# Performance work log

Hardware: AMD Instinct MI355X
Metric: run time of the kernel (lower is better)

The kernel has to match this reference:

```python
import jax, jax.numpy as jnp
import numpy as np

B, S, D, K = 4, 8192, 512, 20


def setup_inputs() -> dict:
    key = jax.random.key(0)
    k1, k2, k3, k4 = jax.random.split(key, 4)
    std = 0.02  # _init_weights: normal(0, 0.02/sqrt(layer_idx+1)), layer_idx=0
    return {
        "x": jax.random.normal(k1, (B, S, D), dtype=jnp.float32),
        "positions": jax.random.normal(k2, (K, D), dtype=jnp.float32) * 0.2,
        "log_scales": jnp.log(1.0 + 0.5 * jax.random.uniform(k3, (K,), dtype=jnp.float32)),
        "amplitudes": 1.2 + 0.3 * jax.random.uniform(k4, (K,), dtype=jnp.float32),
        "w_v": jax.random.normal(jax.random.fold_in(key, 10), (D, D), dtype=jnp.float32) * std,
        "w_o": jax.random.normal(jax.random.fold_in(key, 11), (D, D), dtype=jnp.float32) * std,
    }


def reference(x, positions, log_scales, amplitudes, w_v, w_o):
    # Gaussian-splat RBF attention (token -> splat -> token routing).
    scales = jnp.exp(log_scales)  # [K]
    # squared distances ||x - c||^2 via expansion (avoids [B,S,K,D] tensor)
    x2 = jnp.sum(x * x, axis=-1, keepdims=True)           # [B,S,1]
    c2 = jnp.sum(positions * positions, axis=-1)          # [K]
    xc = jnp.einsum('bsd,kd->bsk', x, positions)          # [B,S,K]
    d2 = jnp.maximum(x2 - 2.0 * xc + c2, 0.0)             # [B,S,K]
    gauss = amplitudes * jnp.exp(-0.5 * d2 / (scales * scales))  # [B,S,K]
    attn = gauss / (jnp.sum(gauss, axis=-1, keepdims=True) + 1e-8)  # per-token normalize
    v = jnp.einsum('bsd,ed->bse', x, w_v)                 # token_value_proj (no bias)
    splat_states = jnp.einsum('bsk,bsd->bkd', attn, v)    # gather token values at splats
    out = jnp.einsum('bsk,bkd->bsd', attn, splat_states)  # scatter back to tokens
    return jnp.einsum('bsd,ed->bse', out, w_o)            # output_proj (dropout=eval identity)
```

## Files before the change

### kernel.cpp

```cpp
#include <hip/hip_runtime.h>
#include <hip/hip_bf16.h>

#define BB 4
#define SS 8192
#define DD 512
#define KK 20
#define CHUNKS 64

__global__ void k0_params(const float* __restrict__ pos,
                          const float* __restrict__ log_scales,
                          const float* __restrict__ amps,
                          float* __restrict__ params) {
  int k = blockIdx.x;
  int lane = threadIdx.x;
  float acc = 0.f;
  for (int d = lane; d < DD; d += 64) { float p = pos[k * DD + d]; acc += p * p; }
#pragma unroll
  for (int off = 32; off > 0; off >>= 1) acc += __shfl_xor(acc, off);
  if (lane == 0) {
    params[k] = acc;
    float s = __expf(log_scales[k]);
    params[KK + k] = 0.5f / (s * s);
    params[2 * KK + k] = amps[k];
  }
}

__global__ __launch_bounds__(256) void k1_attn(
    const float* __restrict__ x, const float* __restrict__ pos,
    const float* __restrict__ params, float* __restrict__ attn) {
  __shared__ float pos_s[KK * DD];
  int tid = threadIdx.x;
  for (int i = tid; i < KK * DD / 4; i += 256)
    ((float4*)pos_s)[i] = ((const float4*)pos)[i];
  __syncthreads();

  int tl = tid >> 2;
  int dsub = tid & 3;
  size_t tok = (size_t)blockIdx.x * 64 + tl;
  const float* xrow = x + tok * DD;

  float acc[KK];
#pragma unroll
  for (int k = 0; k < KK; ++k) acc[k] = 0.f;
  float x2 = 0.f;

#pragma unroll 4
  for (int j = 0; j < 32; ++j) {
    int d0 = j * 16 + dsub * 4;
    float4 xv = *(const float4*)(xrow + d0);
    x2 += xv.x * xv.x + xv.y * xv.y + xv.z * xv.z + xv.w * xv.w;
#pragma unroll
    for (int k = 0; k < KK; ++k) {
      float4 p = *(const float4*)(pos_s + k * DD + d0);
      acc[k] += xv.x * p.x + xv.y * p.y + xv.z * p.z + xv.w * p.w;
    }
  }
#pragma unroll
  for (int k = 0; k < KK; ++k) {
    acc[k] += __shfl_xor(acc[k], 1);
    acc[k] += __shfl_xor(acc[k], 2);
  }
  x2 += __shfl_xor(x2, 1);
  x2 += __shfl_xor(x2, 2);

  if (dsub == 0) {
    float g[KK];
    float sum = 0.f;
#pragma unroll
    for (int k = 0; k < KK; ++k) {
      float d2 = fmaxf(x2 - 2.f * acc[k] + params[k], 0.f);
      float gk = params[2 * KK + k] * __expf(-params[KK + k] * d2);
      g[k] = gk;
      sum += gk;
    }
    float inv = 1.f / (sum + 1e-8f);
    float* arow = attn + tok * KK;
#pragma unroll
    for (int k = 0; k < KK; ++k) arow[k] = g[k] * inv;
  }
}

__global__ __launch_bounds__(256) void k2_scatter(
    const float* __restrict__ x, const float* __restrict__ attn,
    float* __restrict__ Mpart) {
  int t = threadIdx.x;
  int c = blockIdx.x;
  int b = blockIdx.y;
  int s0 = c * (SS / CHUNKS);

  float2 Ml[KK];
#pragma unroll
  for (int k = 0; k < KK; ++k) Ml[k] = make_float2(0.f, 0.f);

  for (int s = s0; s < s0 + SS / CHUNKS; ++s) {
    size_t tokb = (size_t)b * SS + s;
    float2 xv = *(const float2*)(x + tokb * DD + 2 * t);
    const float* arow = attn + tokb * KK;
#pragma unroll
    for (int k = 0; k < KK; ++k) {
      float a = arow[k];
      Ml[k].x += a * xv.x;
      Ml[k].y += a * xv.y;
    }
  }
  float* base = Mpart + (((size_t)b * CHUNKS + c) * KK) * DD + 2 * t;
#pragma unroll
  for (int k = 0; k < KK; ++k)
    *(float2*)(base + (size_t)k * DD) = Ml[k];
}

__global__ __launch_bounds__(256) void k2b_reduce(
    const float* __restrict__ Mpart, float* __restrict__ Mg) {
  int idx = blockIdx.x * 256 + threadIdx.x;
  int b = idx / (KK * DD);
  int kd = idx - b * (KK * DD);
  const float* p = Mpart + (size_t)b * CHUNKS * KK * DD + kd;
  float acc = 0.f;
#pragma unroll 8
  for (int c = 0; c < CHUNKS; ++c) acc += p[(size_t)c * KK * DD];
  Mg[idx] = acc;
}

__global__ __launch_bounds__(256) void k3_proj(
    const float* __restrict__ in, const float* __restrict__ W,
    float* __restrict__ out) {
  __shared__ float row_s[DD];
  int bk = blockIdx.x;
  int t = threadIdx.x;
  for (int i = t; i < DD / 4; i += 256)
    ((float4*)row_s)[i] = ((const float4*)(in + (size_t)bk * DD))[i];
  __syncthreads();
  int e = blockIdx.y * 256 + t;
  const float* wrow = W + (size_t)e * DD;
  float acc = 0.f;
#pragma unroll 4
  for (int j = 0; j < DD / 4; ++j) {
    float4 w4 = *(const float4*)(wrow + 4 * j);
    float4 m4 = ((const float4*)row_s)[j];
    acc += m4.x * w4.x + m4.y * w4.y + m4.z * w4.z + m4.w * w4.w;
  }
  out[(size_t)bk * DD + e] = acc;
}

__global__ __launch_bounds__(256) void k5_gather(
    const float* __restrict__ attn, const float* __restrict__ ws2,
    float* __restrict__ out) {
  int t = threadIdx.x;
  int b = blockIdx.y;
  int s0 = blockIdx.x * (SS / CHUNKS);

  float2 w[KK];
#pragma unroll
  for (int k = 0; k < KK; ++k)
    w[k] = *(const float2*)(ws2 + ((size_t)b * KK + k) * DD + 2 * t);

  for (int s = s0; s < s0 + SS / CHUNKS; ++s) {
    size_t tokb = (size_t)b * SS + s;
    const float* arow = attn + tokb * KK;
    float2 o = make_float2(0.f, 0.f);
#pragma unroll
    for (int k = 0; k < KK; ++k) {
      float a = arow[k];
      o.x += a * w[k].x;
      o.y += a * w[k].y;
    }
    *(float2*)(out + tokb * DD + 2 * t) = o;
  }
}

extern "C" void kernel_launch(void* const* d_in, const int* in_sizes, int n_in,
                              void* d_out, int out_size, void* d_ws, size_t ws_size,
                              hipStream_t stream) {
  const float* x   = (const float*)d_in[0];
  const float* pos = (const float*)d_in[1];
  const float* ls  = (const float*)d_in[2];
  const float* am  = (const float*)d_in[3];
  const float* w_v = (const float*)d_in[4];
  const float* w_o = (const float*)d_in[5];
  float* out = (float*)d_out;

  float* ws     = (float*)d_ws;
  float* params = ws;
  float* attn   = ws + 64;
  float* Mg     = attn + (size_t)BB * SS * KK;
  float* ssb    = Mg + (size_t)BB * KK * DD;
  float* ws2    = ssb + (size_t)BB * KK * DD;
  float* Mpart  = ws2 + (size_t)BB * KK * DD;

  k0_params<<<KK, 64, 0, stream>>>(pos, ls, am, params);
  k1_attn<<<(BB * SS) / 64, 256, 0, stream>>>(x, pos, params, attn);
  k2_scatter<<<dim3(CHUNKS, BB), 256, 0, stream>>>(x, attn, Mpart);
  k2b_reduce<<<(BB * KK * DD) / 256, 256, 0, stream>>>(Mpart, Mg);
  k3_proj<<<dim3(BB * KK, 2), 256, 0, stream>>>(Mg, w_v, ssb);
  k3_proj<<<dim3(BB * KK, 2), 256, 0, stream>>>(ssb, w_o, ws2);
  k5_gather<<<dim3(CHUNKS, BB), 256, 0, stream>>>(attn, ws2, out);
}
```

Measured before the change: 250.6 us.

## Fuse attention, scatter and projections into fewer kernels with per-tile partials

Merges the parameter, attention and scatter stages into one kernel that computes splat weights for 64-token tiles in shared memory, then immediately accumulates per-tile splat partial sums from the same x rows. The two projections and the chunk reduction are folded into a single 512-thread kernel, and the gather kernel now stages attention rows in shared memory with more, smaller blocks. This cuts kernel launches and avoids a second full read of x for the scatter. In exchange it writes many more partial sums (128 chunks per batch), and keeps a fallback path for when the workspace is too small.

```diff
diff --git a/kernel.cpp b/kernel.cpp
--- a/kernel.cpp
+++ b/kernel.cpp
@@ -5,166 +5,231 @@
 #define SS 8192
 #define DD 512
 #define KK 20
-#define CHUNKS 64
-
-__global__ void k0_params(const float* __restrict__ pos,
-                          const float* __restrict__ log_scales,
-                          const float* __restrict__ amps,
-                          float* __restrict__ params) {
-  int k = blockIdx.x;
-  int lane = threadIdx.x;
-  float acc = 0.f;
-  for (int d = lane; d < DD; d += 64) { float p = pos[k * DD + d]; acc += p * p; }
-#pragma unroll
-  for (int off = 32; off > 0; off >>= 1) acc += __shfl_xor(acc, off);
-  if (lane == 0) {
-    params[k] = acc;
-    float s = __expf(log_scales[k]);
-    params[KK + k] = 0.5f / (s * s);
-    params[2 * KK + k] = amps[k];
-  }
-}
-
-__global__ __launch_bounds__(256) void k1_attn(
+#define TT 64
+#define CPB1 (SS / TT)
+#define CPB2 64
+
+__device__ __forceinline__ float dot4(float4 a, float4 b) {
+  return a.x * b.x + a.y * b.y + a.z * b.z + a.w * b.w;
+}
+
+__global__ __launch_bounds__(256) void k12_fused(
     const float* __restrict__ x, const float* __restrict__ pos,
-    const float* __restrict__ params, float* __restrict__ attn) {
+    const float* __restrict__ log_scales, const float* __restrict__ amps,
+    float* __restrict__ attn_g, float* __restrict__ Mpart, int doM) {
   __shared__ float pos_s[KK * DD];
+  __shared__ float attn_s[TT * KK];
+  __shared__ float prm_s[3 * KK];
+
   int tid = threadIdx.x;
+  int blk = blockIdx.x;
+  int b = blk >> 7;
+  int c = blk & 127;
+  size_t row0 = (size_t)b * SS + (size_t)c * TT;
+
   for (int i = tid; i < KK * DD / 4; i += 256)
     ((float4*)pos_s)[i] = ((const float4*)pos)[i];
   __syncthreads();
 
-  int tl = tid >> 2;
-  int dsub = tid & 3;
-  size_t tok = (size_t)blockIdx.x * 64 + tl;
-  const float* xrow = x + tok * DD;
-
-  float acc[KK];
-#pragma unroll
-  for (int k = 0; k < KK; ++k) acc[k] = 0.f;
-  float x2 = 0.f;
-
-#pragma unroll 4
-  for (int j = 0; j < 32; ++j) {
-    int d0 = j * 16 + dsub * 4;
-    float4 xv = *(const float4*)(xrow + d0);
-    x2 += xv.x * xv.x + xv.y * xv.y + xv.z * xv.z + xv.w * xv.w;
+  if (tid < KK * 8) {
+    int k = tid >> 3, i = tid & 7;
+    float a = 0.f;
+    const float4* pr = (const float4*)(pos_s + k * DD);
+#pragma unroll
+    for (int j = 0; j < 16; ++j) {
+      float4 p = pr[i * 16 + j];
+      a += dot4(p, p);
+    }
+    a += __shfl_xor(a, 1); a += __shfl_xor(a, 2); a += __shfl_xor(a, 4);
+    if (i == 0) {
+      prm_s[k] = a;
+      float s = __expf(log_scales[k]);
+      prm_s[KK + k] = 0.5f / (s * s);
+      prm_s[2 * KK + k] = amps[k];
+    }
+  }
+  __syncthreads();
+
+  int q = tid >> 4;
+  int dsub = tid & 15;
+  const float* xq = x + (row0 + q) * DD;
+
+  float acc[4][KK];
+  float x2[4];
+#pragma unroll
+  for (int r = 0; r < 4; ++r) {
+    x2[r] = 0.f;
+#pragma unroll
+    for (int k = 0; k < KK; ++k) acc[r][k] = 0.f;
+  }
+
+  for (int j = 0; j < 8; ++j) {
+    int d0 = j * 64 + dsub * 4;
+    float4 xv[4];
+#pragma unroll
+    for (int r = 0; r < 4; ++r) xv[r] = *(const float4*)(xq + (size_t)r * 16 * DD + d0);
+#pragma unroll
+    for (int r = 0; r < 4; ++r) x2[r] += dot4(xv[r], xv[r]);
 #pragma unroll
     for (int k = 0; k < KK; ++k) {
       float4 p = *(const float4*)(pos_s + k * DD + d0);
-      acc[k] += xv.x * p.x + xv.y * p.y + xv.z * p.z + xv.w * p.w;
-    }
-  }
-#pragma unroll
-  for (int k = 0; k < KK; ++k) {
-    acc[k] += __shfl_xor(acc[k], 1);
-    acc[k] += __shfl_xor(acc[k], 2);
-  }
-  x2 += __shfl_xor(x2, 1);
-  x2 += __shfl_xor(x2, 2);
+#pragma unroll
+      for (int r = 0; r < 4; ++r) acc[r][k] += dot4(xv[r], p);
+    }
+  }
+
+#pragma unroll
+  for (int r = 0; r < 4; ++r) {
+    x2[r] += __shfl_xor(x2[r], 1); x2[r] += __shfl_xor(x2[r], 2);
+    x2[r] += __shfl_xor(x2[r], 4); x2[r] += __shfl_xor(x2[r], 8);
+#pragma unroll
+    for (int k = 0; k < KK; ++k) {
+      float v = acc[r][k];
+      v += __shfl_xor(v, 1); v += __shfl_xor(v, 2);
+      v += __shfl_xor(v, 4); v += __shfl_xor(v, 8);
+      acc[r][k] = v;
+    }
+  }
 
   if (dsub == 0) {
-    float g[KK];
-    float sum = 0.f;
-#pragma unroll
-    for (int k = 0; k < KK; ++k) {
-      float d2 = fmaxf(x2 - 2.f * acc[k] + params[k], 0.f);
-      float gk = params[2 * KK + k] * __expf(-params[KK + k] * d2);
-      g[k] = gk;
-      sum += gk;
-    }
-    float inv = 1.f / (sum + 1e-8f);
-    float* arow = attn + tok * KK;
-#pragma unroll
-    for (int k = 0; k < KK; ++k) arow[k] = g[k] * inv;
-  }
-}
-
-__global__ __launch_bounds__(256) void k2_scatter(
+#pragma unroll
+    for (int r = 0; r < 4; ++r) {
+      float g[KK];
+      float sum = 0.f;
+#pragma unroll
+      for (int k = 0; k < KK; ++k) {
+        float d2 = fmaxf(x2[r] - 2.f * acc[r][k] + prm_s[k], 0.f);
+        float gk = prm_s[2 * KK + k] * __expf(-prm_s[KK + k] * d2);
+        g[k] = gk;
+        sum += gk;
+      }
+      float inv = 1.f / (sum + 1e-8f);
+      float* as = attn_s + (q + r * 16) * KK;
+#pragma unroll
+      for (int k = 0; k < KK; ++k) as[k] = g[k] * inv;
+    }
+  }
+  __syncthreads();
+
+  {
+    float* ag = attn_g + row0 * KK;
+    for (int i = tid; i < TT * KK; i += 256) ag[i] = attn_s[i];
+  }
+
+  if (!doM) return;
+
+  float2 Ml[KK];
+#pragma unroll
+  for (int k = 0; k < KK; ++k) Ml[k] = make_float2(0.f, 0.f);
+
+  const float* xb = x + row0 * DD + 2 * tid;
+  for (int s = 0; s < TT; ++s) {
+    float2 xv = *(const float2*)(xb + (size_t)s * DD);
+    const float4* ar4 = (const float4*)(attn_s + s * KK);
+#pragma unroll
+    for (int kk = 0; kk < KK / 4; ++kk) {
+      float4 a4 = ar4[kk];
+      Ml[4 * kk + 0].x += a4.x * xv.x; Ml[4 * kk + 0].y += a4.x * xv.y;
+      Ml[4 * kk + 1].x += a4.y * xv.x; Ml[4 * kk + 1].y += a4.y * xv.y;
+      Ml[4 * kk + 2].x += a4.z * xv.x; Ml[4 * kk + 2].y += a4.z * xv.y;
+      Ml[4 * kk + 3].x += a4.w * xv.x; Ml[4 * kk + 3].y += a4.w * xv.y;
+    }
+  }
+  float* mp = Mpart + (size_t)blk * KK * DD + 2 * tid;
+#pragma unroll
+  for (int k = 0; k < KK; ++k) *(float2*)(mp + (size_t)k * DD) = Ml[k];
+}
+
+__global__ __launch_bounds__(256) void k2_fb(
     const float* __restrict__ x, const float* __restrict__ attn,
     float* __restrict__ Mpart) {
   int t = threadIdx.x;
   int c = blockIdx.x;
   int b = blockIdx.y;
-  int s0 = c * (SS / CHUNKS);
+  int s0 = c * (SS / CPB2);
 
   float2 Ml[KK];
 #pragma unroll
   for (int k = 0; k < KK; ++k) Ml[k] = make_float2(0.f, 0.f);
 
-  for (int s = s0; s < s0 + SS / CHUNKS; ++s) {
+  for (int s = s0; s < s0 + SS / CPB2; ++s) {
     size_t tokb = (size_t)b * SS + s;
     float2 xv = *(const float2*)(x + tokb * DD + 2 * t);
-    const float* arow = attn + tokb * KK;
-#pragma unroll
-    for (int k = 0; k < KK; ++k) {
-      float a = arow[k];
-      Ml[k].x += a * xv.x;
-      Ml[k].y += a * xv.y;
-    }
-  }
-  float* base = Mpart + (((size_t)b * CHUNKS + c) * KK) * DD + 2 * t;
-#pragma unroll
-  for (int k = 0; k < KK; ++k)
-    *(float2*)(base + (size_t)k * DD) = Ml[k];
-}
-
-__global__ __launch_bounds__(256) void k2b_reduce(
-    const float* __restrict__ Mpart, float* __restrict__ Mg) {
-  int idx = blockIdx.x * 256 + threadIdx.x;
-  int b = idx / (KK * DD);
-  int kd = idx - b * (KK * DD);
-  const float* p = Mpart + (size_t)b * CHUNKS * KK * DD + kd;
+    const float4* ar4 = (const float4*)(attn + tokb * KK);
+#pragma unroll
+    for (int kk = 0; kk < KK / 4; ++kk) {
+      float4 a4 = ar4[kk];
+      Ml[4 * kk + 0].x += a4.x * xv.x; Ml[4 * kk + 0].y += a4.x * xv.y;
+      Ml[4 * kk + 1].x += a4.y * xv.x; Ml[4 * kk + 1].y += a4.y * xv.y;
+      Ml[4 * kk + 2].x += a4.z * xv.x; Ml[4 * kk + 2].y += a4.z * xv.y;
+      Ml[4 * kk + 3].x += a4.w * xv.x; Ml[4 * kk + 3].y += a4.w * xv.y;
+    }
+  }
+  float* base = Mpart + ((size_t)b * CPB2 + c) * KK * DD + 2 * t;
+#pragma unroll
+  for (int k = 0; k < KK; ++k) *(float2*)(base + (size_t)k * DD) = Ml[k];
+}
+
+__global__ __launch_bounds__(512) void k3f(
+    const float* __restrict__ Mpart, const float* __restrict__ w_v,
+    const float* __restrict__ w_o, float* __restrict__ ws2, int cpb) {
+  __shared__ float m_s[DD];
+  __shared__ float v_s[DD];
+  int bk = blockIdx.x;
+  int b = bk / KK, k = bk - b * KK;
+  int e = threadIdx.x;
+
+  const float* mp = Mpart + ((size_t)b * cpb) * KK * DD + (size_t)k * DD + e;
   float acc = 0.f;
 #pragma unroll 8
-  for (int c = 0; c < CHUNKS; ++c) acc += p[(size_t)c * KK * DD];
-  Mg[idx] = acc;
-}
-
-__global__ __launch_bounds__(256) void k3_proj(
-    const float* __restrict__ in, const float* __restrict__ W,
-    float* __restrict__ out) {
-  __shared__ float row_s[DD];
-  int bk = blockIdx.x;
-  int t = threadIdx.x;
-  for (int i = t; i < DD / 4; i += 256)
-    ((float4*)row_s)[i] = ((const float4*)(in + (size_t)bk * DD))[i];
-  __syncthreads();
-  int e = blockIdx.y * 256 + t;
-  const float* wrow = W + (size_t)e * DD;
-  float acc = 0.f;
+  for (int c = 0; c < cpb; ++c) acc += mp[(size_t)c * KK * DD];
+  m_s[e] = acc;
+  __syncthreads();
+
+  const float4* wr = (const float4*)(w_v + (size_t)e * DD);
+  float a2 = 0.f;
 #pragma unroll 4
-  for (int j = 0; j < DD / 4; ++j) {
-    float4 w4 = *(const float4*)(wrow + 4 * j);
-    float4 m4 = ((const float4*)row_s)[j];
-    acc += m4.x * w4.x + m4.y * w4.y + m4.z * w4.z + m4.w * w4.w;
-  }
-  out[(size_t)bk * DD + e] = acc;
+  for (int j = 0; j < DD / 4; ++j) a2 += dot4(((const float4*)m_s)[j], wr[j]);
+  v_s[e] = a2;
+  __syncthreads();
+
+  const float4* wr2 = (const float4*)(w_o + (size_t)e * DD);
+  float a3 = 0.f;
+#pragma unroll 4
+  for (int j = 0; j < DD / 4; ++j) a3 += dot4(((const float4*)v_s)[j], wr2[j]);
+  ws2[(size_t)bk * DD + e] = a3;
 }
 
 __global__ __launch_bounds__(256) void k5_gather(
     const float* __restrict__ attn, const float* __restrict__ ws2,
     float* __restrict__ out) {
-  int t = threadIdx.x;
+  __shared__ float a_s[32 * KK];
+  int tid = threadIdx.x;
   int b = blockIdx.y;
-  int s0 = blockIdx.x * (SS / CHUNKS);
+  int s0 = blockIdx.x * 32;
+
+  const float* ab = attn + ((size_t)b * SS + s0) * KK;
+  for (int i = tid; i < 32 * KK; i += 256) a_s[i] = ab[i];
 
   float2 w[KK];
-#pragma unroll
-  for (int k = 0; k < KK; ++k)
-    w[k] = *(const float2*)(ws2 + ((size_t)b * KK + k) * DD + 2 * t);
-
-  for (int s = s0; s < s0 + SS / CHUNKS; ++s) {
-    size_t tokb = (size_t)b * SS + s;
-    const float* arow = attn + tokb * KK;
+  const float* wb = ws2 + (size_t)b * KK * DD + 2 * tid;
+#pragma unroll
+  for (int k = 0; k < KK; ++k) w[k] = *(const float2*)(wb + (size_t)k * DD);
+  __syncthreads();
+
+  float* ob = out + ((size_t)b * SS + s0) * DD + 2 * tid;
+  for (int s = 0; s < 32; ++s) {
+    const float4* ar4 = (const float4*)(a_s + s * KK);
     float2 o = make_float2(0.f, 0.f);
 #pragma unroll
-    for (int k = 0; k < KK; ++k) {
-      float a = arow[k];
-      o.x += a * w[k].x;
-      o.y += a * w[k].y;
-    }
-    *(float2*)(out + tokb * DD + 2 * t) = o;
+    for (int kk = 0; kk < KK / 4; ++kk) {
+      float4 a4 = ar4[kk];
+      o.x += a4.x * w[4 * kk + 0].x; o.y += a4.x * w[4 * kk + 0].y;
+      o.x += a4.y * w[4 * kk + 1].x; o.y += a4.y * w[4 * kk + 1].y;
+      o.x += a4.z * w[4 * kk + 2].x; o.y += a4.z * w[4 * kk + 2].y;
+      o.x += a4.w * w[4 * kk + 3].x; o.y += a4.w * w[4 * kk + 3].y;
+    }
+    *(float2*)(ob + (size_t)s * DD) = o;
   }
 }
 
@@ -179,19 +244,21 @@
   const float* w_o = (const float*)d_in[5];
   float* out = (float*)d_out;
 
-  float* ws     = (float*)d_ws;
-  float* params = ws;
-  float* attn   = ws + 64;
-  float* Mg     = attn + (size_t)BB * SS * KK;
-  float* ssb    = Mg + (size_t)BB * KK * DD;
-  float* ws2    = ssb + (size_t)BB * KK * DD;
-  float* Mpart  = ws2 + (size_t)BB * KK * DD;
-
-  k0_params<<<KK, 64, 0, stream>>>(pos, ls, am, params);
-  k1_attn<<<(BB * SS) / 64, 256, 0, stream>>>(x, pos, params, attn);
-  k2_scatter<<<dim3(CHUNKS, BB), 256, 0, stream>>>(x, attn, Mpart);
-  k2b_reduce<<<(BB * KK * DD) / 256, 256, 0, stream>>>(Mpart, Mg);
-  k3_proj<<<dim3(BB * KK, 2), 256, 0, stream>>>(Mg, w_v, ssb);
-  k3_proj<<<dim3(BB * KK, 2), 256, 0, stream>>>(ssb, w_o, ws2);
-  k5_gather<<<dim3(CHUNKS, BB), 256, 0, stream>>>(attn, ws2, out);
-}
+  float* ws   = (float*)d_ws;
+  float* attn = ws;
+  float* ws2  = attn + (size_t)BB * SS * KK;
+  float* Mpart = ws2 + (size_t)BB * KK * DD;
+
+  size_t need_fused = ((size_t)BB * SS * KK + (size_t)BB * KK * DD +
+                       (size_t)BB * CPB1 * KK * DD) * sizeof(float);
+
+  if (ws_size >= need_fused) {
+    k12_fused<<<BB * SS / TT, 256, 0, stream>>>(x, pos, ls, am, attn, Mpart, 1);
+    k3f<<<BB * KK, 512, 0, stream>>>(Mpart, w_v, w_o, ws2, CPB1);
+  } else {
+    k12_fused<<<BB * SS / TT, 256, 0, stream>>>(x, pos, ls, am, attn, Mpart, 0);
+    k2_fb<<<dim3(CPB2, BB), 256, 0, stream>>>(x, attn, Mpart);
+    k3f<<<BB * KK, 512, 0, stream>>>(Mpart, w_v, w_o, ws2, CPB2);
+  }
+  k5_gather<<<dim3(SS / 32, BB), 256, 0, stream>>>(attn, ws2, out);
+}
```

Measured after the change: 255.4 us. About the same (+1.9%).
